# Kernel tuning notes

Measured on AMD Instinct MI355X. Metric: run time of the kernel, lower is better.

The kernel has to match this reference:

```python
import jax, jax.numpy as jnp
import numpy as np

B, N, CIN, H, E = 1, 20000, 128, 128, 320000


def setup_inputs() -> dict:
    key = jax.random.key(0)
    ks = jax.random.split(key, 16)
    x = jax.random.normal(ks[0], (B, N, CIN), jnp.float32)
    edge_index = jax.random.randint(ks[1], (2, E), 0, N, dtype=jnp.int64)
    edge_weight = jax.random.uniform(ks[2], (E,), jnp.float32)
    h = jax.random.normal(ks[3], (B, N, H), jnp.float32)
    c = jax.random.normal(ks[4], (B, N, H), jnp.float32)
    # GCN stack params, gate order [i, f, c, o]; 2 layers each (K=2)
    Wx0 = jax.random.normal(ks[5], (4, CIN, H), jnp.float32) / np.float32(np.sqrt(CIN))
    bx0 = jnp.zeros((4, H), jnp.float32)
    Wx1 = jax.random.normal(ks[6], (4, H, H), jnp.float32) / np.float32(np.sqrt(H))
    bx1 = jnp.zeros((4, H), jnp.float32)
    Wh0 = jax.random.normal(ks[7], (4, H, H), jnp.float32) / np.float32(np.sqrt(H))
    bh0 = jnp.zeros((4, H), jnp.float32)
    Wh1 = jax.random.normal(ks[8], (4, H, H), jnp.float32) / np.float32(np.sqrt(H))
    bh1 = jnp.zeros((4, H), jnp.float32)
    wc = jax.random.normal(ks[9], (3, H), jnp.float32) * 0.1  # peephole [i, f, o]
    bg = jnp.zeros((4, H), jnp.float32)  # gate biases [i, f, c, o]
    return dict(x=x, edge_index=edge_index, edge_weight=edge_weight, h=h, c=c,
                Wx0=Wx0, bx0=bx0, Wx1=Wx1, bx1=bx1,
                Wh0=Wh0, bh0=bh0, Wh1=Wh1, bh1=bh1, wc=wc, bg=bg)


def reference(x, edge_index, edge_weight, h, c,
              Wx0, bx0, Wx1, bx1, Wh0, bh0, Wh1, bh1, wc, bg):
    n = x.shape[1]
    src, dst = edge_index[0], edge_index[1]
    loop = jnp.arange(n)
    src2 = jnp.concatenate([src, loop])
    dst2 = jnp.concatenate([dst, loop])
    w2 = jnp.concatenate([edge_weight, jnp.ones((n,), edge_weight.dtype)])
    deg = jax.ops.segment_sum(w2, dst2, num_segments=n)
    dis = jnp.where(deg > 0, jax.lax.rsqrt(jnp.maximum(deg, 1e-12)), 0.0)
    norm = dis[src2] * w2 * dis[dst2]  # sym GCN norm with self loops

    def prop(t):  # t: [..., N, F] -> D^-1/2 (A+I) D^-1/2 t
        lead = t.shape[:-2]
        tf = t.reshape((-1,) + t.shape[-2:])
        m = tf[:, src2, :] * norm[None, :, None]
        agg = jax.vmap(lambda mm: jax.ops.segment_sum(mm, dst2, num_segments=n))(m)
        return agg.reshape(lead + agg.shape[-2:])

    def gcn4(t, W0, b0, W1, b1):  # 2-layer GCN, 4 gates at once
        a = prop(t)  # shared first aggregation: [B,N,F]
        h0 = jax.nn.relu(jnp.einsum('bnc,gch->gbnh', a, W0) + b0[:, None, None, :])
        a1 = prop(h0)  # [4,B,N,H]
        return jnp.einsum('gbnh,ghk->gbnk', a1, W1) + b1[:, None, None, :]

    G = gcn4(x, Wx0, bx0, Wx1, bx1) + gcn4(h, Wh0, bh0, Wh1, bh1)  # [4,B,N,H]
    I = jax.nn.sigmoid(G[0] + wc[0] * c + bg[0])
    F = jax.nn.sigmoid(G[1] + wc[1] * c + bg[1])
    T = jnp.tanh(G[2] + bg[2])
    Cn = F * c + I * T
    O = jax.nn.sigmoid(G[3] + wc[2] * Cn + bg[3])
    Hn = O * jnp.tanh(Cn)
    return (Hn, Cn)
```

## Files before the change

### kernel.cpp

```cpp
#include <hip/hip_runtime.h>
#include <hip/hip_bf16.h>
#include <stdint.h>

#define NN    20000
#define NP    20096
#define EE    320000
#define CH    128
#define GC    512
#define NHtot 2560000

typedef short bf16x8 __attribute__((ext_vector_type(8)));
typedef float f32x4  __attribute__((ext_vector_type(4)));

__device__ __forceinline__ unsigned short f2bf(float f) {
    __hip_bfloat16 b = __float2bfloat16(f);
    union { __hip_bfloat16 b; unsigned short u; } c; c.b = b; return c.u;
}
__device__ __forceinline__ void fma8(uint4 u, float n, float* acc) {
    union { unsigned int i; float f; } t;
    t.i = u.x << 16;         acc[0] += n * t.f;
    t.i = u.x & 0xffff0000u; acc[1] += n * t.f;
    t.i = u.y << 16;         acc[2] += n * t.f;
    t.i = u.y & 0xffff0000u; acc[3] += n * t.f;
    t.i = u.z << 16;         acc[4] += n * t.f;
    t.i = u.z & 0xffff0000u; acc[5] += n * t.f;
    t.i = u.w << 16;         acc[6] += n * t.f;
    t.i = u.w & 0xffff0000u; acc[7] += n * t.f;
}
__device__ __forceinline__ void tof8(uint4 u, float* f) {
    union { unsigned int i; float f; } t;
    t.i = u.x << 16;         f[0] = t.f;
    t.i = u.x & 0xffff0000u; f[1] = t.f;
    t.i = u.y << 16;         f[2] = t.f;
    t.i = u.y & 0xffff0000u; f[3] = t.f;
    t.i = u.z << 16;         f[4] = t.f;
    t.i = u.z & 0xffff0000u; f[5] = t.f;
    t.i = u.w << 16;         f[6] = t.f;
    t.i = u.w & 0xffff0000u; f[7] = t.f;
}
__device__ __forceinline__ uint2 pack4(const float* f) {
    uint2 v;
    v.x = (unsigned int)f2bf(f[0]) | ((unsigned int)f2bf(f[1]) << 16);
    v.y = (unsigned int)f2bf(f[2]) | ((unsigned int)f2bf(f[3]) << 16);
    return v;
}
__device__ __forceinline__ void gload_lds16(const void* g, void* l) {
    __builtin_amdgcn_global_load_lds(
        (const __attribute__((address_space(1))) void*)g,
        (__attribute__((address_space(3))) void*)l, 16, 0, 0);
}

__global__ void k_cntprep(const int* __restrict__ ei, int* __restrict__ cnt,
                          const float* __restrict__ W0, const float* __restrict__ W1,
                          const float* __restrict__ W2, const float* __restrict__ W3,
                          unsigned short* __restrict__ T0, unsigned short* __restrict__ T1,
                          unsigned short* __restrict__ T2, unsigned short* __restrict__ T3,
                          const float* __restrict__ bx1, const float* __restrict__ bh1,
                          const float* __restrict__ bg, float* __restrict__ btot) {
    int bid = blockIdx.x;
    if (bid < EE / 256) {
        int e = bid * 256 + threadIdx.x;
        atomicAdd(&cnt[ei[EE + e]], 1);
        return;
    }
    int pid = bid - EE / 256;
    int z = pid >> 8, y = (pid >> 6) & 3, xb = pid & 63;
    if (z == 0 && y == 0 && xb < 2) {
        int f = xb * 256 + threadIdx.x;
        btot[f] = bx1[f] + bh1[f] + bg[f];
    }
    const float* W; unsigned short* T;
    switch (z) {
        case 0:  W = W0; T = T0; break;
        case 1:  W = W1; T = T1; break;
        case 2:  W = W2; T = T2; break;
        default: W = W3; T = T3; break;
    }
    int n = xb * 2 + (threadIdx.x >> 7);
    int k = threadIdx.x & 127;
    T[((size_t)y * 128 + n) * 128 + k] = f2bf(W[((size_t)y * 128 + k) * 128 + n]);
}

__global__ void k_scan1(const int* __restrict__ cnt, int* __restrict__ rowoff,
                        int* __restrict__ bsum) {
    __shared__ int wsum[4];
    int i = blockIdx.x * 256 + threadIdx.x;
    int self = (i < NN) ? cnt[i] : 0;
    int lane = threadIdx.x & 63, wid = threadIdx.x >> 6;
    int v = self;
    #pragma unroll
    for (int off = 1; off < 64; off <<= 1) {
        int u = __shfl_up(v, off);
        if (lane >= off) v += u;
    }
    if (lane == 63) wsum[wid] = v;
    __syncthreads();
    int wof = 0;
    for (int k = 0; k < wid; ++k) wof += wsum[k];
    if (i < NN) rowoff[i] = wof + v - self;
    if (threadIdx.x == 255) bsum[blockIdx.x] = wof + v;
}

__global__ void k_scan2(int* __restrict__ bsum) {
    int lane = threadIdx.x;
    int base = 0;
    for (int start = 0; start < 80; start += 64) {
        int i = start + lane;
        int self = (i < 80) ? bsum[i] : 0;
        int v = self;
        #pragma unroll
        for (int off = 1; off < 64; off <<= 1) {
            int u = __shfl_up(v, off);
            if (lane >= off) v += u;
        }
        if (i < 80) bsum[i] = base + v - self;
        base += __shfl(v, 63);
    }
}

__global__ void k_scan3(int* __restrict__ rowoff, const int* __restrict__ bsum,
                        int* __restrict__ cur) {
    int i = blockIdx.x * 256 + threadIdx.x;
    if (i < NN) {
        int v = rowoff[i] + bsum[i >> 8];
        rowoff[i] = v; cur[i] = v;
    }
    if (i == NN) rowoff[NN] = EE;
}

__global__ void k_scatter(const int* __restrict__ ei, const float* __restrict__ ew,
                          int* __restrict__ cur,
                          int* __restrict__ csrs, float* __restrict__ csrw) {
    int e = blockIdx.x * 256 + threadIdx.x;
    if (e >= EE) return;
    int s = ei[e], d = ei[EE + e];
    int p = atomicAdd(&cur[d], 1);
    csrs[p] = s; csrw[p] = ew[e];
}

__global__ __launch_bounds__(256) void k_degcast(
        const float* __restrict__ x, const float* __restrict__ h,
        const int* __restrict__ rowoff, const float* __restrict__ csrw,
        float* __restrict__ dis, unsigned short* __restrict__ xhb) {
    int wid = threadIdx.x >> 6, lane = threadIdx.x & 63;
    int w = blockIdx.x * 4 + wid;
    int e0 = rowoff[w], e1 = rowoff[w + 1];
    float s = 0.f;
    for (int e = e0 + lane; e < e1; e += 64) s += csrw[e];
    #pragma unroll
    for (int off = 32; off; off >>= 1) s += __shfl_xor(s, off);
    float dn = rsqrtf(fmaxf(1.0f + s, 1e-12f));
    if (lane == 0) dis[w] = dn;
    const float* src = (lane < 32) ? x + (size_t)w * CH + lane * 4
                                   : h + (size_t)w * CH + (lane - 32) * 4;
    float4 v = *(const float4*)src;
    float f[4] = { dn * v.x, dn * v.y, dn * v.z, dn * v.w };
    *(uint2*)(xhb + (size_t)w * 256 + lane * 4) = pack4(f);
}

__global__ __launch_bounds__(256) void k_prop256c(
        const unsigned short* __restrict__ tab, unsigned short* __restrict__ o,
        const int* __restrict__ rowoff, const int* __restrict__ csrs,
        const float* __restrict__ csrw, const float* __restrict__ dis) {
    int chunk = blockIdx.x & 3;
    int w = (blockIdx.x >> 2) * 4 + (threadIdx.x >> 6);
    int l = threadIdx.x & 63, grp = l >> 3, li = l & 7;
    const uint4* T4 = (const uint4*)tab;
    int coff = chunk * 8 + li;
    float acc[8];
    #pragma unroll
    for (int j = 0; j < 8; ++j) acc[j] = 0.f;
    if (grp == 0) tof8(T4[(size_t)w * 32 + coff], acc);
    int e = rowoff[w], e1 = rowoff[w + 1];
    for (; e + 16 <= e1; e += 16) {
        int   sA = csrs[e + grp],  sB = csrs[e + 8 + grp];
        float nA = csrw[e + grp],  nB = csrw[e + 8 + grp];
        uint4 uA = T4[(size_t)sA * 32 + coff];
        uint4 uB = T4[(size_t)sB * 32 + coff];
        fma8(uA, nA, acc); fma8(uB, nB, acc);
    }
    for (; e + 8 <= e1; e += 8) {
        int s = csrs[e + grp]; float n = csrw[e + grp];
        fma8(T4[(size_t)s * 32 + coff], n, acc);
    }
    if (grp < e1 - e) {
        int s = csrs[e + grp]; float n = csrw[e + grp];
        fma8(T4[(size_t)s * 32 + coff], n, acc);
    }
    #pragma unroll
    for (int j = 0; j < 8; ++j) {
        acc[j] += __shfl_xor(acc[j], 8);
        acc[j] += __shfl_xor(acc[j], 16);
        acc[j] += __shfl_xor(acc[j], 32);
    }
    if (grp == 0) {
        float dw = dis[w];
        #pragma unroll
        for (int j = 0; j < 8; ++j) acc[j] *= dw;
        uint2 p0 = pack4(acc), p1 = pack4(acc + 4);
        uint4 ov; ov.x = p0.x; ov.y = p0.y; ov.z = p1.x; ov.w = p1.y;
        ((uint4*)o)[(size_t)w * 32 + coff] = ov;
    }
}

#define SWZ(r, c8) (((r) << 4) + ((c8) ^ ((r) & 15)))

__global__ __launch_bounds__(256) void k_gemm1(
        const unsigned short* __restrict__ A,
        const unsigned short* __restrict__ Wtx, const unsigned short* __restrict__ Wth,
        const float* __restrict__ bx0, const float* __restrict__ bh0,
        unsigned short* __restrict__ outx, unsigned short* __restrict__ outh) {
    __shared__ uint4 As[2048];
    __shared__ uint4 Bs[2048];
    const int side = blockIdx.z;
    const int aoff = side * 128;
    const unsigned short* Wt = side ? Wth : Wtx;
    const float* bias        = side ? bh0 : bx0;
    unsigned short* out      = side ? outh : outx;

    const int    g    = blockIdx.y;
    const size_t row0 = (size_t)blockIdx.x * 128;
    const int    t    = threadIdx.x;
    const int    wv   = t >> 6;
    const unsigned short* Wg = Wt + (size_t)g * 16384;

    #pragma unroll
    for (int p = 0; p < 8; ++p) {
        int id = t + 256 * p, r = id >> 4, cc = id & 15;
        int c8 = cc ^ (r & 15);
        gload_lds16(A + (row0 + r) * 256 + aoff + c8 * 8, &As[p * 256 + wv * 64]);
        gload_lds16(Wg + r * CH + c8 * 8,                 &Bs[p * 256 + wv * 64]);
    }
    __syncthreads();

    const int l = t & 63;
    const int m0 = (wv >> 1) * 64, n0 = (wv & 1) * 64;
    const int lm = l & 15, q = l >> 4;
    f32x4 acc[4][4];
    #pragma unroll
    for (int i = 0; i < 4; ++i)
        #pragma unroll
        for (int j = 0; j < 4; ++j) { acc[i][j][0]=0.f; acc[i][j][1]=0.f; acc[i][j][2]=0.f; acc[i][j][3]=0.f; }

    #pragma unroll
    for (int kc = 0; kc < 4; ++kc) {
        int c8 = kc * 4 + q;
        bf16x8 a[4], b[4];
        #pragma unroll
        for (int i = 0; i < 4; ++i) { int r = m0 + i * 16 + lm; a[i] = *(const bf16x8*)&As[SWZ(r, c8)]; }
        #pragma unroll
        for (int j = 0; j < 4; ++j) { int r = n0 + j * 16 + lm; b[j] = *(const bf16x8*)&Bs[SWZ(r, c8)]; }
        #pragma unroll
        for (int i = 0; i < 4; ++i)
            #pragma unroll
            for (int j = 0; j < 4; ++j)
                acc[i][j] = __builtin_amdgcn_mfma_f32_16x16x32_bf16(a[i], b[j], acc[i][j], 0, 0, 0);
    }

    #pragma unroll
    for (int j = 0; j < 4; ++j) {
        float bb = bias[g * CH + n0 + j * 16 + lm];
        #pragma unroll
        for (int i = 0; i < 4; ++i)
            #pragma unroll
            for (int r = 0; r < 4; ++r) {
                int rowl = m0 + i * 16 + q * 4 + r;
                int col  = n0 + j * 16 + lm;
                out[(row0 + rowl) * GC + g * CH + col] = f2bf(fmaxf(acc[i][j][r] + bb, 0.f));
            }
    }
}

__global__ __launch_bounds__(256) void k_gemm2(
        const unsigned short* __restrict__ A1, const unsigned short* __restrict__ A2,
        const unsigned short* __restrict__ Wt1, const unsigned short* __restrict__ Wt2,
        const float* __restrict__ dis, unsigned short* __restrict__ outS) {
    __shared__ uint4 As[2048];
    __shared__ uint4 Bs[2048];
    const int    g    = blockIdx.y;
    const size_t row0 = (size_t)blockIdx.x * 128;
    const int    t    = threadIdx.x;
    const int    wv   = t >> 6;
    const int l = t & 63;
    const int m0 = (wv >> 1) * 64, n0 = (wv & 1) * 64;
    const int lm = l & 15, q = l >> 4;
    f32x4 acc[4][4];
    #pragma unroll
    for (int i = 0; i < 4; ++i)
        #pragma unroll
        for (int j = 0; j < 4; ++j) { acc[i][j][0]=0.f; acc[i][j][1]=0.f; acc[i][j][2]=0.f; acc[i][j][3]=0.f; }

    for (int side = 0; side < 2; ++side) {
        if (side) __syncthreads();
        const unsigned short* Ap = side ? A2 : A1;
        const unsigned short* Wg = (side ? Wt2 : Wt1) + (size_t)g * 16384;
        #pragma unroll
        for (int p = 0; p < 8; ++p) {
            int id = t + 256 * p, r = id >> 4, cc = id & 15;
            int c8 = cc ^ (r & 15);
            gload_lds16(Ap + (row0 + r) * GC + g * CH + c8 * 8, &As[p * 256 + wv * 64]);
            gload_lds16(Wg + r * CH + c8 * 8,                   &Bs[p * 256 + wv * 64]);
        }
        __syncthreads();
        #pragma unroll
        for (int kc = 0; kc < 4; ++kc) {
            int c8 = kc * 4 + q;
            bf16x8 a[4], b[4];
            #pragma unroll
            for (int i = 0; i < 4; ++i) { int r = m0 + i * 16 + lm; a[i] = *(const bf16x8*)&As[SWZ(r, c8)]; }
            #pragma unroll
            for (int j = 0; j < 4; ++j) { int r = n0 + j * 16 + lm; b[j] = *(const bf16x8*)&Bs[SWZ(r, c8)]; }
            #pragma unroll
            for (int i = 0; i < 4; ++i)
                #pragma unroll
                for (int j = 0; j < 4; ++j)
                    acc[i][j] = __builtin_amdgcn_mfma_f32_16x16x32_bf16(a[i], b[j], acc[i][j], 0, 0, 0);
        }
    }

    #pragma unroll
    for (int j = 0; j < 4; ++j) {
        int fh = (n0 + j * 16) >> 4;
        #pragma unroll
        for (int i = 0; i < 4; ++i)
            #pragma unroll
            for (int r = 0; r < 4; ++r) {
                int rowl = m0 + i * 16 + q * 4 + r;
                float dr = dis[row0 + rowl];
                outS[(row0 + rowl) * GC + fh * 64 + g * 16 + lm] = f2bf(dr * acc[i][j][r]);
            }
    }
}

__global__ __launch_bounds__(256) void k_prop512w(
        const unsigned short* __restrict__ Sb, float* __restrict__ Gbuf,
        const int* __restrict__ rowoff, const int* __restrict__ csrs,
        const float* __restrict__ csrw, const float* __restrict__ dis) {
    int chunk = blockIdx.x & 7;
    int w = (blockIdx.x >> 3) * 4 + (threadIdx.x >> 6);
    int l = threadIdx.x & 63, grp = l >> 3, li = l & 7;
    const uint4* S4 = (const uint4*)Sb;
    int coff = chunk * 8 + li;
    float acc[8];
    #pragma unroll
    for (int j = 0; j < 8; ++j) acc[j] = 0.f;
    if (grp == 0) tof8(S4[(size_t)w * 64 + coff], acc);
    int e = rowoff[w], e1 = rowoff[w + 1];
    for (; e + 16 <= e1; e += 16) {
        int   sA = csrs[e + grp],  sB = csrs[e + 8 + grp];
        float nA = csrw[e + grp],  nB = csrw[e + 8 + grp];
        uint4 uA = S4[(size_t)sA * 64 + coff];
        uint4 uB = S4[(size_t)sB * 64 + coff];
        fma8(uA, nA, acc); fma8(uB, nB, acc);
    }
    for (; e + 8 <= e1; e += 8) {
        int s = csrs[e + grp]; float n = csrw[e + grp];
        fma8(S4[(size_t)s * 64 + coff], n, acc);
    }
    if (grp < e1 - e) {
        int s = csrs[e + grp]; float n = csrw[e + grp];
        fma8(S4[(size_t)s * 64 + coff], n, acc);
    }
    #pragma unroll
    for (int j = 0; j < 8; ++j) {
        acc[j] += __shfl_xor(acc[j], 8);
        acc[j] += __shfl_xor(acc[j], 16);
        acc[j] += __shfl_xor(acc[j], 32);
    }
    if (grp == 0) {
        float dw = dis[w];
        #pragma unroll
        for (int j = 0; j < 8; ++j) acc[j] *= dw;
        float* gp = Gbuf + (size_t)w * GC + chunk * 64 + li * 8;
        *(float4*)gp       = *(float4*)&acc[0];
        *(float4*)(gp + 4) = *(float4*)&acc[4];
    }
}

__global__ __launch_bounds__(256) void k_lstm(
        const float* __restrict__ Gbuf, const float* __restrict__ c,
        const float* __restrict__ btot, const float* __restrict__ wc,
        float* __restrict__ out) {
    int t = threadIdx.x;
    int w = blockIdx.x * 2 + (t >> 7);
    int hh = t & 127;
    const float* gr = Gbuf + (size_t)w * GC + ((hh >> 4) << 6) + (hh & 15);
    float g0 = gr[0]  + btot[hh];
    float g1 = gr[16] + btot[128 + hh];
    float g2 = gr[32] + btot[256 + hh];
    float g3 = gr[48] + btot[384 + hh];
    float cv = c[(size_t)w * CH + hh];
    float I  = 1.f / (1.f + expf(-(g0 + wc[hh]       * cv)));
    float F  = 1.f / (1.f + expf(-(g1 + wc[128 + hh] * cv)));
    float T  = tanhf(g2);
    float Cn = F * cv + I * T;
    float O  = 1.f / (1.f + expf(-(g3 + wc[256 + hh] * Cn)));
    out[(size_t)w * CH + hh]         = O * tanhf(Cn);
    out[NHtot + (size_t)w * CH + hh] = Cn;
}

extern "C" void kernel_launch(void* const* d_in, const int* in_sizes, int n_in,
                              void* d_out, int out_size, void* d_ws, size_t ws_size,
                              hipStream_t stream) {
    (void)in_sizes; (void)n_in; (void)out_size; (void)ws_size;
    const float* x   = (const float*)d_in[0];
    const int*   ei  = (const int*)d_in[1];
    const float* ew  = (const float*)d_in[2];
    const float* h   = (const float*)d_in[3];
    const float* c   = (const float*)d_in[4];
    const float* Wx0 = (const float*)d_in[5];
    const float* bx0 = (const float*)d_in[6];
    const float* Wx1 = (const float*)d_in[7];
    const float* bx1 = (const float*)d_in[8];
    const float* Wh0 = (const float*)d_in[9];
    const float* bh0 = (const float*)d_in[10];
    const float* Wh1 = (const float*)d_in[11];
    const float* bh1 = (const float*)d_in[12];
    const float* wc  = (const float*)d_in[13];
    const float* bg  = (const float*)d_in[14];
    float* out = (float*)d_out;

    float* wsf  = (float*)d_ws;
    float* dis  = wsf;
    int*   cnt  = (int*)(wsf + 20480);
    int*   row  = (int*)(wsf + 40960);
    int*   cur  = (int*)(wsf + 61696);
    int*   bsum = (int*)(wsf + 82176);
    float* btot = wsf + 82432;
    int*   csrs = (int*)(wsf + 82944);
    float* csrw = wsf + 402944;
    unsigned short* Wt0x = (unsigned short*)(wsf + 722944);
    unsigned short* Wt0h = (unsigned short*)(wsf + 755712);
    unsigned short* Wt1x = (unsigned short*)(wsf + 788480);
    unsigned short* Wt1h = (unsigned short*)(wsf + 821248);
    unsigned short* xhb  = (unsigned short*)(wsf + 854016);
    unsigned short* axh  = (unsigned short*)(wsf + 3426304);
    unsigned short* h0x  = (unsigned short*)(wsf + 5998592);
    unsigned short* h0h  = (unsigned short*)(wsf + 11143168);
    unsigned short* Sb   = (unsigned short*)(wsf + 16287744);
    float* Gbuf = wsf + 5998592;

    hipMemsetAsync(cnt, 0, 20480 * sizeof(int), stream);

    k_cntprep<<<EE / 256 + 1024, 256, 0, stream>>>(ei, cnt,
                                                   Wx0, Wh0, Wx1, Wh1,
                                                   Wt0x, Wt0h, Wt1x, Wt1h,
                                                   bx1, bh1, bg, btot);
    k_scan1  <<<80, 256, 0, stream>>>(cnt, row, bsum);
    k_scan2  <<<1, 64, 0, stream>>>(bsum);
    k_scan3  <<<80, 256, 0, stream>>>(row, bsum, cur);
    k_scatter<<<EE / 256, 256, 0, stream>>>(ei, ew, cur, csrs, csrw);

    k_degcast<<<NN / 4, 256, 0, stream>>>(x, h, row, csrw, dis, xhb);

    k_prop256c<<<(NN / 4) * 4, 256, 0, stream>>>(xhb, axh, row, csrs, csrw, dis);

    dim3 g1(NP / 128, 4, 2);
    k_gemm1<<<g1, 256, 0, stream>>>(axh, Wt0x, Wt0h, bx0, bh0, h0x, h0h);
    dim3 g2(NP / 128, 4);
    k_gemm2<<<g2, 256, 0, stream>>>(h0x, h0h, Wt1x, Wt1h, dis, Sb);

    k_prop512w<<<(NN / 4) * 8, 256, 0, stream>>>(Sb, Gbuf, row, csrs, csrw, dis);
    k_lstm<<<NN / 2, 256, 0, stream>>>(Gbuf, c, btot, wc, out);
}
```

Measured before the change: 293.0 us.

## Assign one node per 8-lane group in propagation kernels, drop cross-group reductions

```diff
diff --git a/kernel.cpp b/kernel.cpp
--- a/kernel.cpp
+++ b/kernel.cpp
@@ -42,6 +42,14 @@
     uint2 v;
     v.x = (unsigned int)f2bf(f[0]) | ((unsigned int)f2bf(f[1]) << 16);
     v.y = (unsigned int)f2bf(f[2]) | ((unsigned int)f2bf(f[3]) << 16);
+    return v;
+}
+__device__ __forceinline__ uint4 pack8(const float* f) {
+    uint4 v;
+    v.x = (unsigned int)f2bf(f[0]) | ((unsigned int)f2bf(f[1]) << 16);
+    v.y = (unsigned int)f2bf(f[2]) | ((unsigned int)f2bf(f[3]) << 16);
+    v.z = (unsigned int)f2bf(f[4]) | ((unsigned int)f2bf(f[5]) << 16);
+    v.w = (unsigned int)f2bf(f[6]) | ((unsigned int)f2bf(f[7]) << 16);
     return v;
 }
 __device__ __forceinline__ void gload_lds16(const void* g, void* l) {
@@ -158,49 +166,44 @@
     *(uint2*)(xhb + (size_t)w * 256 + lane * 4) = pack4(f);
 }
 
-__global__ __launch_bounds__(256) void k_prop256c(
+__global__ __launch_bounds__(256) void k_prop256m(
         const unsigned short* __restrict__ tab, unsigned short* __restrict__ o,
         const int* __restrict__ rowoff, const int* __restrict__ csrs,
         const float* __restrict__ csrw, const float* __restrict__ dis) {
     int chunk = blockIdx.x & 3;
-    int w = (blockIdx.x >> 2) * 4 + (threadIdx.x >> 6);
+    int wbase = (blockIdx.x >> 2) * 32 + (threadIdx.x >> 6) * 8;
     int l = threadIdx.x & 63, grp = l >> 3, li = l & 7;
+    int w = wbase + grp;
     const uint4* T4 = (const uint4*)tab;
     int coff = chunk * 8 + li;
     float acc[8];
-    #pragma unroll
-    for (int j = 0; j < 8; ++j) acc[j] = 0.f;
-    if (grp == 0) tof8(T4[(size_t)w * 32 + coff], acc);
-    int e = rowoff[w], e1 = rowoff[w + 1];
-    for (; e + 16 <= e1; e += 16) {
-        int   sA = csrs[e + grp],  sB = csrs[e + 8 + grp];
-        float nA = csrw[e + grp],  nB = csrw[e + 8 + grp];
-        uint4 uA = T4[(size_t)sA * 32 + coff];
-        uint4 uB = T4[(size_t)sB * 32 + coff];
-        fma8(uA, nA, acc); fma8(uB, nB, acc);
-    }
-    for (; e + 8 <= e1; e += 8) {
-        int s = csrs[e + grp]; float n = csrw[e + grp];
+    tof8(T4[(size_t)w * 32 + coff], acc);
+    int e0 = rowoff[w], deg = rowoff[w + 1] - e0;
+    int md = deg;
+    md = max(md, __shfl_xor(md, 8));
+    md = max(md, __shfl_xor(md, 16));
+    md = max(md, __shfl_xor(md, 32));
+    int k = 0;
+    for (; k + 2 <= md; k += 2) {
+        bool a0 = k < deg, a1 = k + 1 < deg;
+        int i0 = a0 ? e0 + k : 0, i1 = a1 ? e0 + k + 1 : 0;
+        int s0 = csrs[i0], s1 = csrs[i1];
+        float n0 = a0 ? csrw[i0] : 0.f;
+        float n1 = a1 ? csrw[i1] : 0.f;
+        uint4 u0 = T4[(size_t)s0 * 32 + coff];
+        uint4 u1 = T4[(size_t)s1 * 32 + coff];
+        fma8(u0, n0, acc); fma8(u1, n1, acc);
+    }
+    if (k < md) {
+        bool a = k < deg;
+        int i0 = a ? e0 + k : 0;
+        int s = csrs[i0]; float n = a ? csrw[i0] : 0.f;
         fma8(T4[(size_t)s * 32 + coff], n, acc);
     }
-    if (grp < e1 - e) {
-        int s = csrs[e + grp]; float n = csrw[e + grp];
-        fma8(T4[(size_t)s * 32 + coff], n, acc);
-    }
-    #pragma unroll
-    for (int j = 0; j < 8; ++j) {
-        acc[j] += __shfl_xor(acc[j], 8);
-        acc[j] += __shfl_xor(acc[j], 16);
-        acc[j] += __shfl_xor(acc[j], 32);
-    }
-    if (grp == 0) {
-        float dw = dis[w];
-        #pragma unroll
-        for (int j = 0; j < 8; ++j) acc[j] *= dw;
-        uint2 p0 = pack4(acc), p1 = pack4(acc + 4);
-        uint4 ov; ov.x = p0.x; ov.y = p0.y; ov.z = p1.x; ov.w = p1.y;
-        ((uint4*)o)[(size_t)w * 32 + coff] = ov;
-    }
+    float dw = dis[w];
+    #pragma unroll
+    for (int j = 0; j < 8; ++j) acc[j] *= dw;
+    ((uint4*)o)[(size_t)w * 32 + coff] = pack8(acc);
 }
 
 #define SWZ(r, c8) (((r) << 4) + ((c8) ^ ((r) & 15)))
@@ -319,62 +322,58 @@
     }
 
     #pragma unroll
-    for (int j = 0; j < 4; ++j) {
-        int fh = (n0 + j * 16) >> 4;
+    for (int j = 0; j < 4; ++j)
         #pragma unroll
         for (int i = 0; i < 4; ++i)
             #pragma unroll
             for (int r = 0; r < 4; ++r) {
                 int rowl = m0 + i * 16 + q * 4 + r;
+                int col  = n0 + j * 16 + lm;
                 float dr = dis[row0 + rowl];
-                outS[(row0 + rowl) * GC + fh * 64 + g * 16 + lm] = f2bf(dr * acc[i][j][r]);
+                outS[(row0 + rowl) * GC + g * CH + col] = f2bf(dr * acc[i][j][r]);
             }
-    }
-}
-
-__global__ __launch_bounds__(256) void k_prop512w(
+}
+
+__global__ __launch_bounds__(256) void k_prop512m(
         const unsigned short* __restrict__ Sb, float* __restrict__ Gbuf,
         const int* __restrict__ rowoff, const int* __restrict__ csrs,
         const float* __restrict__ csrw, const float* __restrict__ dis) {
     int chunk = blockIdx.x & 7;
-    int w = (blockIdx.x >> 3) * 4 + (threadIdx.x >> 6);
+    int wbase = (blockIdx.x >> 3) * 32 + (threadIdx.x >> 6) * 8;
     int l = threadIdx.x & 63, grp = l >> 3, li = l & 7;
+    int w = wbase + grp;
     const uint4* S4 = (const uint4*)Sb;
     int coff = chunk * 8 + li;
     float acc[8];
-    #pragma unroll
-    for (int j = 0; j < 8; ++j) acc[j] = 0.f;
-    if (grp == 0) tof8(S4[(size_t)w * 64 + coff], acc);
-    int e = rowoff[w], e1 = rowoff[w + 1];
-    for (; e + 16 <= e1; e += 16) {
-        int   sA = csrs[e + grp],  sB = csrs[e + 8 + grp];
-        float nA = csrw[e + grp],  nB = csrw[e + 8 + grp];
-        uint4 uA = S4[(size_t)sA * 64 + coff];
-        uint4 uB = S4[(size_t)sB * 64 + coff];
-        fma8(uA, nA, acc); fma8(uB, nB, acc);
-    }
-    for (; e + 8 <= e1; e += 8) {
-        int s = csrs[e + grp]; float n = csrw[e + grp];
+    tof8(S4[(size_t)w * 64 + coff], acc);
+    int e0 = rowoff[w], deg = rowoff[w + 1] - e0;
+    int md = deg;
+    md = max(md, __shfl_xor(md, 8));
+    md = max(md, __shfl_xor(md, 16));
+    md = max(md, __shfl_xor(md, 32));
+    int k = 0;
+    for (; k + 2 <= md; k += 2) {
+        bool a0 = k < deg, a1 = k + 1 < deg;
+        int i0 = a0 ? e0 + k : 0, i1 = a1 ? e0 + k + 1 : 0;
+        int s0 = csrs[i0], s1 = csrs[i1];
+        float n0 = a0 ? csrw[i0] : 0.f;
+        float n1 = a1 ? csrw[i1] : 0.f;
+        uint4 u0 = S4[(size_t)s0 * 64 + coff];
+        uint4 u1 = S4[(size_t)s1 * 64 + coff];
+        fma8(u0, n0, acc); fma8(u1, n1, acc);
+    }
+    if (k < md) {
+        bool a = k < deg;
+        int i0 = a ? e0 + k : 0;
+        int s = csrs[i0]; float n = a ? csrw[i0] : 0.f;
         fma8(S4[(size_t)s * 64 + coff], n, acc);
     }
-    if (grp < e1 - e) {
-        int s = csrs[e + grp]; float n = csrw[e + grp];
-        fma8(S4[(size_t)s * 64 + coff], n, acc);
-    }
-    #pragma unroll
-    for (int j = 0; j < 8; ++j) {
-        acc[j] += __shfl_xor(acc[j], 8);
-        acc[j] += __shfl_xor(acc[j], 16);
-        acc[j] += __shfl_xor(acc[j], 32);
-    }
-    if (grp == 0) {
-        float dw = dis[w];
-        #pragma unroll
-        for (int j = 0; j < 8; ++j) acc[j] *= dw;
-        float* gp = Gbuf + (size_t)w * GC + chunk * 64 + li * 8;
-        *(float4*)gp       = *(float4*)&acc[0];
-        *(float4*)(gp + 4) = *(float4*)&acc[4];
-    }
+    float dw = dis[w];
+    #pragma unroll
+    for (int j = 0; j < 8; ++j) acc[j] *= dw;
+    float* gp = Gbuf + (size_t)w * GC + chunk * 64 + li * 8;
+    *(float4*)gp       = *(float4*)&acc[0];
+    *(float4*)(gp + 4) = *(float4*)&acc[4];
 }
 
 __global__ __launch_bounds__(256) void k_lstm(
@@ -384,11 +383,11 @@
     int t = threadIdx.x;
     int w = blockIdx.x * 2 + (t >> 7);
     int hh = t & 127;
-    const float* gr = Gbuf + (size_t)w * GC + ((hh >> 4) << 6) + (hh & 15);
-    float g0 = gr[0]  + btot[hh];
-    float g1 = gr[16] + btot[128 + hh];
-    float g2 = gr[32] + btot[256 + hh];
-    float g3 = gr[48] + btot[384 + hh];
+    const float* gr = Gbuf + (size_t)w * GC;
+    float g0 = gr[hh]       + btot[hh];
+    float g1 = gr[128 + hh] + btot[128 + hh];
+    float g2 = gr[256 + hh] + btot[256 + hh];
+    float g3 = gr[384 + hh] + btot[384 + hh];
     float cv = c[(size_t)w * CH + hh];
     float I  = 1.f / (1.f + expf(-(g0 + wc[hh]       * cv)));
     float F  = 1.f / (1.f + expf(-(g1 + wc[128 + hh] * cv)));
@@ -453,13 +452,13 @@
 
     k_degcast<<<NN / 4, 256, 0, stream>>>(x, h, row, csrw, dis, xhb);
 
-    k_prop256c<<<(NN / 4) * 4, 256, 0, stream>>>(xhb, axh, row, csrs, csrw, dis);
+    k_prop256m<<<(NN / 32) * 4, 256, 0, stream>>>(xhb, axh, row, csrs, csrw, dis);
 
     dim3 g1(NP / 128, 4, 2);
     k_gemm1<<<g1, 256, 0, stream>>>(axh, Wt0x, Wt0h, bx0, bh0, h0x, h0h);
     dim3 g2(NP / 128, 4);
     k_gemm2<<<g2, 256, 0, stream>>>(h0x, h0h, Wt1x, Wt1h, dis, Sb);
 
-    k_prop512w<<<(NN / 4) * 8, 256, 0, stream>>>(Sb, Gbuf, row, csrs, csrw, dis);
+    k_prop512m<<<(NN / 32) * 8, 256, 0, stream>>>(Sb, Gbuf, row, csrs, csrw, dis);
     k_lstm<<<NN / 2, 256, 0, stream>>>(Gbuf, c, btot, wc, out);
 }
```

Measured after the change: 259.0 us. -11.6%, faster.
